# Optimization experiments

Measured on AMD Instinct MI355X. Metric: run time of the kernel, lower is better.

The kernel has to match this reference:

```python
import jax, jax.numpy as jnp
import numpy as np

H = 64; H2 = 32; B = 256; NPART = 64
NP = B * NPART          # 16384 part nodes
PER_TF = 512            # torque/force nodes per graph
NT = B * PER_TF; NF = NT
E = 262144              # edges per edge type
L = 5; T = 4            # 4 main hetero layers + 1 actor layer; 4 edge types
NEG = 0.2; EPS = 1e-5


def _seg_softmax(e, seg, n):
    # softmax over entries sharing the same segment id (along axis 0)
    m = jax.lax.stop_gradient(jax.ops.segment_max(e, seg, num_segments=n))
    ex = jnp.exp(e - m[seg])
    s = jax.ops.segment_sum(ex, seg, num_segments=n)
    return ex / s[seg]


def _gat(x_s, x_d, es, ed, Ws, Wd, a_s, a_d, b, n_dst):
    # PyG GATConv, heads=1, add_self_loops=False, bipartite (x_src, x_dst)
    hs = x_s @ Ws                      # [Ns,H]
    hd = x_d @ Wd                      # [Nd,H]
    e = jax.nn.leaky_relu((hs @ a_s)[es] + (hd @ a_d)[ed], NEG)   # [E]
    al = _seg_softmax(e, ed, n_dst)                                # attn per dst neighborhood
    return jax.ops.segment_sum(al[:, None] * hs[es], ed, num_segments=n_dst) + b


def _hetero_layer(xp, xt, xf, edges, Ws, Wd, a_s, a_d, b):
    # to_hetero(aggr='sum'): one GATConv per edge type, sum into each dst type
    (pts, ptd), (tps, tpd), (pfs, pfd), (fps, fpd) = edges
    out_t = _gat(xp, xt, pts, ptd, Ws[0], Wd[0], a_s[0], a_d[0], b[0], xt.shape[0])
    out_p = (_gat(xt, xp, tps, tpd, Ws[1], Wd[1], a_s[1], a_d[1], b[1], xp.shape[0])
             + _gat(xf, xp, fps, fpd, Ws[3], Wd[3], a_s[3], a_d[3], b[3], xp.shape[0]))
    out_f = _gat(xp, xf, pfs, pfd, Ws[2], Wd[2], a_s[2], a_d[2], b[2], xf.shape[0])
    return out_p, out_t, out_f


def _pool(x):
    # MultiAggregation([max, min, mean]); segments are uniform -> reshape
    xr = x.reshape(B, -1, x.shape[-1])
    return jnp.concatenate([xr.max(1), xr.min(1), xr.mean(1)], axis=-1)


def reference(mass, part_state, torque_x, force_x,
              e_pt_src, e_pt_dst, e_tp_src, e_tp_dst,
              e_pf_src, e_pf_dst, e_fp_src, e_fp_dst,
              batch, part_id,
              emb_parts_W, emb_state, W_src, W_dst, a_src, a_dst, b_conv,
              ln_gamma, ln_beta, out_a_W, out_a_b,
              innet_W, innet_b, full_W, full_b, outnet_W, outnet_b):
    edges = ((e_pt_src, e_pt_dst), (e_tp_src, e_tp_dst),
             (e_pf_src, e_pf_dst), (e_fp_src, e_fp_dst))
    idx = part_state[:, 0] + 2 * part_state[:, 1]
    xp = jnp.concatenate([mass @ emb_parts_W, emb_state[idx]], axis=-1)  # [NP,H]
    xt, xf = torque_x, force_x
    for l in range(4):  # main hetero GAT, ReLU between layers, none after last
        xp, xt, xf = _hetero_layer(xp, xt, xf, edges,
                                   W_src[l], W_dst[l], a_src[l], a_dst[l], b_conv[l])
        if l < 3:
            xp, xt, xf = jax.nn.relu(xp), jax.nn.relu(xt), jax.nn.relu(xf)
    # actor: 1-layer hetero GAT (no activation)
    ap, at, af = _hetero_layer(xp, xt, xf, edges,
                               W_src[4], W_dst[4], a_src[4], a_dst[4], b_conv[4])
    # node LayerNorm
    mu = ap.mean(-1, keepdims=True)
    var = ((ap - mu) ** 2).mean(-1, keepdims=True)
    ra = (ap - mu) / jnp.sqrt(var + EPS) * ln_gamma + ln_beta
    ra = ra @ out_a_W + out_a_b                         # [NP,2]
    soft = _seg_softmax(ra, batch, B)                   # softmax per graph, per channel
    actions = jnp.zeros((B, 2, NPART), dtype=ra.dtype).at[batch, :, part_id].set(soft)
    actions = actions.reshape(B, 2 * NPART)
    rep = jnp.concatenate([_pool(xp), _pool(xt), _pool(xf)], axis=1)   # [B, 9H]
    repV = jax.nn.gelu(rep @ innet_W + innet_b, approximate=False)
    repV = jax.nn.gelu(repV @ full_W + full_b, approximate=False)
    V = jnp.tanh(repV @ outnet_W + outnet_b)            # [B,1]
    return actions, V


def setup_inputs():
    key = jax.random.key(0)
    ks = iter(jax.random.split(key, 40))
    f32 = jnp.float32
    inp = {}
    inp['mass'] = jax.random.uniform(next(ks), (NP, 1), dtype=f32)
    inp['part_state'] = jax.random.randint(next(ks), (NP, 2), 0, 2, dtype=jnp.int32)
    inp['torque_x'] = jax.random.normal(next(ks), (NT, H), dtype=f32)
    inp['force_x'] = jax.random.normal(next(ks), (NF, H), dtype=f32)
    for name, n in [('e_pt_src', NP), ('e_pt_dst', NT), ('e_tp_src', NT), ('e_tp_dst', NP),
                    ('e_pf_src', NP), ('e_pf_dst', NF), ('e_fp_src', NF), ('e_fp_dst', NP)]:
        inp[name] = jax.random.randint(next(ks), (E,), 0, n, dtype=jnp.int32)
    inp['batch'] = (jnp.arange(NP) // NPART).astype(jnp.int32)
    inp['part_id'] = (jnp.arange(NP) % NPART).astype(jnp.int32)
    s = 1.0 / np.sqrt(H)
    inp['emb_parts_W'] = jax.random.normal(next(ks), (1, H2), dtype=f32)
    inp['emb_state'] = jax.random.normal(next(ks), (4, H2), dtype=f32)
    inp['W_src'] = jax.random.normal(next(ks), (L, T, H, H), dtype=f32) * s
    inp['W_dst'] = jax.random.normal(next(ks), (L, T, H, H), dtype=f32) * s
    inp['a_src'] = jax.random.normal(next(ks), (L, T, H), dtype=f32) * s
    inp['a_dst'] = jax.random.normal(next(ks), (L, T, H), dtype=f32) * s
    inp['b_conv'] = jax.random.normal(next(ks), (L, T, H), dtype=f32) * 0.01
    inp['ln_gamma'] = jnp.ones((H,), dtype=f32)
    inp['ln_beta'] = jnp.zeros((H,), dtype=f32)
    inp['out_a_W'] = jax.random.normal(next(ks), (H, 2), dtype=f32) * s
    inp['out_a_b'] = jnp.zeros((2,), dtype=f32)
    inp['innet_W'] = jax.random.normal(next(ks), (9 * H, H), dtype=f32) / np.sqrt(9.0 * H)
    inp['innet_b'] = jnp.zeros((H,), dtype=f32)
    inp['full_W'] = jax.random.normal(next(ks), (H, H), dtype=f32) * s
    inp['full_b'] = jnp.zeros((H,), dtype=f32)
    inp['outnet_W'] = jax.random.normal(next(ks), (H, 1), dtype=f32) * s
    inp['outnet_b'] = jnp.zeros((1,), dtype=f32)
    return inp
```

## Files before the change

kernel.cpp:

```cpp
#include <hip/hip_runtime.h>
#include <math.h>

#define NP_ 16384
#define NT_ 131072
#define NF_ 131072
#define E_  262144
#define B_  256
#define NDTOT 294912
#define E4_  1048576

#define D0 0
#define D1 131072
#define D2 147456
#define D3 278528
#define S0 0
#define S1 16384
#define S2 147456
#define S3 163840

typedef float v4f __attribute__((ext_vector_type(4)));

__device__ __forceinline__ float dot4(float4 a, float4 b) {
  return a.x * b.x + a.y * b.y + a.z * b.z + a.w * b.w;
}

__device__ __forceinline__ void nt_store4(float* p, float4 o) {
  v4f v = { o.x, o.y, o.z, o.w };
  __builtin_nontemporal_store(v, (v4f*)p);
}

__device__ __forceinline__ float4 gather_row(int kb, int ke, float ad,
    const int* __restrict__ sortsrc, const float* __restrict__ aS_seg,
    const float* __restrict__ xsrc, int q, int lanebase, float* si_out) {
  float4 acc = make_float4(0.f, 0.f, 0.f, 0.f);
  float m = -3e38f, ssum = 0.f;
  for (int base = kb; base < ke; base += 16) {
    int k = base + q;
    int valid = (k < ke);
    int sidx = valid ? sortsrc[k] : 0;
    float e = -3e38f;
    if (valid) {
      e = aS_seg[sidx] + ad;
      e = e > 0.f ? e : 0.2f * e;
    }
    float cm = e;
#pragma unroll
    for (int off = 1; off < 16; off <<= 1) cm = fmaxf(cm, __shfl_xor(cm, off));
    float mn = fmaxf(m, cm);
    float w = valid ? __expf(e - mn) : 0.f;
    float ws = w;
#pragma unroll
    for (int off = 1; off < 16; off <<= 1) ws += __shfl_xor(ws, off);
    float r = __expf(m - mn);
    ssum = ssum * r + ws;
    acc.x *= r; acc.y *= r; acc.z *= r; acc.w *= r;
    int cnt = min(16, ke - base);
    int i = 0;
    for (; i + 4 <= cnt; i += 4) {
      float w0 = __shfl(w, lanebase + i, 64);
      float w1 = __shfl(w, lanebase + i + 1, 64);
      float w2 = __shfl(w, lanebase + i + 2, 64);
      float w3 = __shfl(w, lanebase + i + 3, 64);
      int s0 = __shfl(sidx, lanebase + i, 64);
      int s1 = __shfl(sidx, lanebase + i + 1, 64);
      int s2 = __shfl(sidx, lanebase + i + 2, 64);
      int s3 = __shfl(sidx, lanebase + i + 3, 64);
      float4 x0 = *(const float4*)(xsrc + (size_t)s0 * 64 + q * 4);
      float4 x1 = *(const float4*)(xsrc + (size_t)s1 * 64 + q * 4);
      float4 x2 = *(const float4*)(xsrc + (size_t)s2 * 64 + q * 4);
      float4 x3 = *(const float4*)(xsrc + (size_t)s3 * 64 + q * 4);
      acc.x += w0 * x0.x + w1 * x1.x + w2 * x2.x + w3 * x3.x;
      acc.y += w0 * x0.y + w1 * x1.y + w2 * x2.y + w3 * x3.y;
      acc.z += w0 * x0.z + w1 * x1.z + w2 * x2.z + w3 * x3.z;
      acc.w += w0 * x0.w + w1 * x1.w + w2 * x2.w + w3 * x3.w;
    }
    for (; i < cnt; i++) {
      float wi = __shfl(w, lanebase + i, 64);
      int si = __shfl(sidx, lanebase + i, 64);
      float4 xv = *(const float4*)(xsrc + (size_t)si * 64 + q * 4);
      acc.x += wi * xv.x; acc.y += wi * xv.y; acc.z += wi * xv.z; acc.w += wi * xv.w;
    }
    m = mn;
  }
  *si_out = (ssum > 0.f) ? 1.f / ssum : 0.f;
  return acc;
}

__global__ void k_wa(const float* __restrict__ Wsrc, const float* __restrict__ Wdst,
                     const float* __restrict__ asrc, const float* __restrict__ adst,
                     float* __restrict__ wsas, float* __restrict__ wdad) {
  int b = blockIdx.x;
  int lt = b >> 1;
  int role = b & 1;
  int k = threadIdx.x;
  const float* W = (role == 0 ? Wsrc : Wdst) + ((size_t)(lt * 64 + k)) * 64;
  const float* a = (role == 0 ? asrc : adst) + lt * 64;
  float s = 0.f;
  for (int i = 0; i < 64; i++) s += W[i] * a[i];
  (role == 0 ? wsas : wdad)[lt * 64 + k] = s;
}

__global__ __launch_bounds__(256) void k_build_xp(const float* __restrict__ mass,
    const int* __restrict__ ps, const float* __restrict__ embW,
    const float* __restrict__ embS, const float* __restrict__ wsas,
    const float* __restrict__ wdad, float* __restrict__ xp,
    float* __restrict__ aS, float* __restrict__ aD) {
  int tid = threadIdx.x;
  int n = blockIdx.x * 16 + (tid >> 4);
  int q = tid & 15;
  float4 v;
  if (q < 8) {
    float mv = mass[n];
    const float* e = embW + q * 4;
    v.x = mv * e[0]; v.y = mv * e[1]; v.z = mv * e[2]; v.w = mv * e[3];
  } else {
    int idx = ps[n * 2] + 2 * ps[n * 2 + 1];
    const float4* e = (const float4*)(embS + idx * 32 + (q - 8) * 4);
    v = *e;
  }
  *(float4*)(xp + (size_t)n * 64 + q * 4) = v;
  float4 w0 = *(const float4*)(wsas + 0 * 64 + q * 4);
  float4 w2 = *(const float4*)(wsas + 2 * 64 + q * 4);
  float4 d1 = *(const float4*)(wdad + 1 * 64 + q * 4);
  float4 d3 = *(const float4*)(wdad + 3 * 64 + q * 4);
  float p0 = dot4(v, w0), p2 = dot4(v, w2), p1 = dot4(v, d1), p3 = dot4(v, d3);
#pragma unroll
  for (int off = 1; off < 16; off <<= 1) {
    p0 += __shfl_xor(p0, off); p2 += __shfl_xor(p2, off);
    p1 += __shfl_xor(p1, off); p3 += __shfl_xor(p3, off);
  }
  if (q == 0) { aS[S0 + n] = p0; aS[S2 + n] = p2; aD[D1 + n] = p1; aD[D3 + n] = p3; }
}

__global__ __launch_bounds__(256) void k_init_dots(const float* __restrict__ tx,
    const float* __restrict__ fx, const float* __restrict__ wsas,
    const float* __restrict__ wdad, float* __restrict__ aS, float* __restrict__ aD) {
  int tid = threadIdx.x;
  int q = tid & 15, slot = tid >> 4;
  int b = blockIdx.x;
  int isF = (b >= 8192);
  int n = (isF ? b - 8192 : b) * 16 + slot;
  const float* src = (isF ? fx : tx) + (size_t)n * 64 + q * 4;
  float4 v = *(const float4*)src;
  int tsrc = isF ? 3 : 1, tdst = isF ? 2 : 0;
  float4 ws = *(const float4*)(wsas + tsrc * 64 + q * 4);
  float4 wd = *(const float4*)(wdad + tdst * 64 + q * 4);
  float pS = dot4(v, ws), pD = dot4(v, wd);
#pragma unroll
  for (int off = 1; off < 16; off <<= 1) {
    pS += __shfl_xor(pS, off); pD += __shfl_xor(pD, off);
  }
  if (q == 0) {
    if (!isF) { aS[S1 + n] = pS; aD[D0 + n] = pD; }
    else      { aS[S3 + n] = pS; aD[D2 + n] = pD; }
  }
}

__global__ __launch_bounds__(256) void k_count(
    const int* __restrict__ d0, const int* __restrict__ d1,
    const int* __restrict__ d2, const int* __restrict__ d3,
    int* __restrict__ counts) {
  __shared__ int cnt[64];
  int b = blockIdx.x;
  int t = b >> 6, c = b & 63;
  const int* dp = (t == 0) ? d0 : (t == 1) ? d1 : (t == 2) ? d2 : d3;
  int sh = (t & 1) ? 8 : 11;
  int tid = threadIdx.x;
  if (tid < 64) cnt[tid] = 0;
  __syncthreads();
  const int4* dp4 = (const int4*)dp + (size_t)c * 1024;
  for (int i = tid; i < 1024; i += 256) {
    int4 v = dp4[i];
    atomicAdd(&cnt[v.x >> sh], 1);
    atomicAdd(&cnt[v.y >> sh], 1);
    atomicAdd(&cnt[v.z >> sh], 1);
    atomicAdd(&cnt[v.w >> sh], 1);
  }
  __syncthreads();
  if (tid < 64) counts[(b << 6) + tid] = cnt[tid];
}

__global__ __launch_bounds__(256) void k_bases(const int* __restrict__ counts,
    int* __restrict__ cbase, int* __restrict__ granBase, int* __restrict__ rowptr) {
  __shared__ int tot[256];
  int tid = threadIdx.x;
  int t = tid >> 6, g = tid & 63;
  int s = 0;
  for (int c = 0; c < 64; c++) s += counts[(((t << 6) | c) << 6) + g];
  tot[tid] = s;
  __syncthreads();
  for (int off = 1; off < 256; off <<= 1) {
    int x = 0; if (tid >= off) x = tot[tid - off];
    __syncthreads(); tot[tid] += x; __syncthreads();
  }
  int gb = tot[tid] - s;
  granBase[tid] = gb;
  if (tid == 255) granBase[256] = E4_;
  if (tid == 0) rowptr[NDTOT] = E4_;
  int run = gb;
  for (int c = 0; c < 64; c++) {
    int idx = (((t << 6) | c) << 6) + g;
    int v = counts[idx];
    cbase[idx] = run;
    run += v;
  }
}

__global__ __launch_bounds__(256) void k_place(
    const int* __restrict__ d0, const int* __restrict__ s0,
    const int* __restrict__ d1, const int* __restrict__ s1,
    const int* __restrict__ d2, const int* __restrict__ s2,
    const int* __restrict__ d3, const int* __restrict__ s3,
    const int* __restrict__ cbase, int2* __restrict__ pairs) {
  __shared__ int cur[64];
  int b = blockIdx.x;
  int t = b >> 6, c = b & 63;
  const int* dp; const int* sp;
  if (t == 0) { dp = d0; sp = s0; }
  else if (t == 1) { dp = d1; sp = s1; }
  else if (t == 2) { dp = d2; sp = s2; }
  else { dp = d3; sp = s3; }
  int sh = (t & 1) ? 8 : 11;
  int tid = threadIdx.x;
  if (tid < 64) cur[tid] = cbase[(b << 6) + tid];
  __syncthreads();
  const int4* dp4 = (const int4*)dp + (size_t)c * 1024;
  const int4* sp4 = (const int4*)sp + (size_t)c * 1024;
  for (int i = tid; i < 1024; i += 256) {
    int4 d = dp4[i];
    int4 s = sp4[i];
    int pos;
    pos = atomicAdd(&cur[d.x >> sh], 1); pairs[pos] = make_int2(d.x, s.x);
    pos = atomicAdd(&cur[d.y >> sh], 1); pairs[pos] = make_int2(d.y, s.y);
    pos = atomicAdd(&cur[d.z >> sh], 1); pairs[pos] = make_int2(d.z, s.z);
    pos = atomicAdd(&cur[d.w >> sh], 1); pairs[pos] = make_int2(d.w, s.w);
  }
}

__global__ __launch_bounds__(256) void k_build(const int2* __restrict__ pairs,
    const int* __restrict__ granBase, int* __restrict__ rowptr,
    int* __restrict__ sortsrc) {
  __shared__ int cnt[2048];
  __shared__ int psum[256];
  int g = blockIdx.x;
  int t = g >> 6, gg = g & 63;
  int rows = (t & 1) ? 256 : 2048;
  int rowLo = gg * rows;
  int csr0;
  if (t == 0) csr0 = D0 + rowLo;
  else if (t == 1) csr0 = D1 + rowLo;
  else if (t == 2) csr0 = D2 + rowLo;
  else csr0 = D3 + rowLo;
  int eb = granBase[g], ee = granBase[g + 1];
  int tid = threadIdx.x;
  for (int i = tid; i < rows; i += 256) cnt[i] = 0;
  __syncthreads();
  for (int i = eb + tid; i < ee; i += 256) {
    int2 p = pairs[i];
    atomicAdd(&cnt[p.x - rowLo], 1);
  }
  __syncthreads();
  int per = rows >> 8;
  int b0 = tid * per;
  int s = 0;
  for (int j = 0; j < per; j++) s += cnt[b0 + j];
  psum[tid] = s;
  __syncthreads();
  for (int off = 1; off < 256; off <<= 1) {
    int x = 0; if (tid >= off) x = psum[tid - off];
    __syncthreads(); psum[tid] += x; __syncthreads();
  }
  int run = psum[tid] - s;
  for (int j = 0; j < per; j++) {
    int v = cnt[b0 + j];
    cnt[b0 + j] = run;
    rowptr[csr0 + b0 + j] = eb + run;
    run += v;
  }
  __syncthreads();
  for (int i = eb + tid; i < ee; i += 256) {
    int2 p = pairs[i];
    int pos = eb + atomicAdd(&cnt[p.x - rowLo], 1);
    sortsrc[pos] = p.y;
  }
}

__global__ __launch_bounds__(256) void k_part_hs(int l, const float* __restrict__ Wsrc,
    const float* __restrict__ bconv, const float* __restrict__ xt,
    const float* __restrict__ xf, const float* __restrict__ xp,
    const int* __restrict__ rowptr, const int* __restrict__ sortsrc,
    const float* __restrict__ aSrd, const float* __restrict__ aDrd,
    float* __restrict__ aSwr, float* __restrict__ aDwr,
    const float* __restrict__ wsas, const float* __restrict__ wdad,
    float* __restrict__ xpo, float* __restrict__ hs0, float* __restrict__ hs2,
    int relu, int writeDots) {
  __shared__ float Wl[4096];
  __shared__ float shC[2176];
  int tid = threadIdx.x;

  if (blockIdx.x >= NP_ / 16) {
    int b = blockIdx.x - NP_ / 16;
    const float4* W0g = (const float4*)(Wsrc + (size_t)(l * 4 + 0) * 4096);
    const float4* W2g = (const float4*)(Wsrc + (size_t)(l * 4 + 2) * 4096);
#pragma unroll
    for (int i = 0; i < 4; i++) ((float4*)Wl)[i * 256 + tid] = W0g[i * 256 + tid];
    int rlocal = tid >> 4, q = tid & 15;
    int n = b * 16 + rlocal;
    float4 xv = *(const float4*)(xp + (size_t)n * 64 + q * 4);
    *(float4*)(shC + rlocal * 68 + q * 4) = xv;
    __syncthreads();
    const float* xr = shC + rlocal * 68;
    const float4* Wc = (const float4*)Wl;
    float4 o0 = make_float4(0.f, 0.f, 0.f, 0.f);
#pragma unroll 4
    for (int k4 = 0; k4 < 16; k4++) {
      float4 a4 = *(const float4*)(xr + k4 * 4);
#pragma unroll
      for (int kk = 0; kk < 4; kk++) {
        float av = kk == 0 ? a4.x : kk == 1 ? a4.y : kk == 2 ? a4.z : a4.w;
        float4 w0 = Wc[(k4 * 4 + kk) * 16 + q];
        o0.x += av * w0.x; o0.y += av * w0.y; o0.z += av * w0.z; o0.w += av * w0.w;
      }
    }
    *(float4*)(hs0 + (size_t)n * 64 + q * 4) = o0;
    __syncthreads();
#pragma unroll
    for (int i = 0; i < 4; i++) ((float4*)Wl)[i * 256 + tid] = W2g[i * 256 + tid];
    __syncthreads();
    float4 o2 = make_float4(0.f, 0.f, 0.f, 0.f);
#pragma unroll 4
    for (int k4 = 0; k4 < 16; k4++) {
      float4 a4 = *(const float4*)(xr + k4 * 4);
#pragma unroll
      for (int kk = 0; kk < 4; kk++) {
        float av = kk == 0 ? a4.x : kk == 1 ? a4.y : kk == 2 ? a4.z : a4.w;
        float4 w2 = Wc[(k4 * 4 + kk) * 16 + q];
        o2.x += av * w2.x; o2.y += av * w2.y; o2.z += av * w2.z; o2.w += av * w2.w;
      }
    }
    *(float4*)(hs2 + (size_t)n * 64 + q * 4) = o2;
    return;
  }

  float* rowA = shC; float* rowB = shC + 1088;
  const float4* W1g = (const float4*)(Wsrc + (size_t)(l * 4 + 1) * 4096);
  const float4* W3g = (const float4*)(Wsrc + (size_t)(l * 4 + 3) * 4096);
#pragma unroll
  for (int i = 0; i < 4; i++) ((float4*)Wl)[i * 256 + tid] = W1g[i * 256 + tid];

  int rlocal = tid >> 4;
  int q = tid & 15;
  int lanebase = (tid & 63) & 48;
  int n = blockIdx.x * 16 + rlocal;
  int row1 = D1 + n;
  int row3 = D3 + n;

  {
    int kb = rowptr[row1], ke = rowptr[row1 + 1];
    float si;
    float4 acc = gather_row(kb, ke, aDrd[row1], sortsrc, aSrd + S1, xt, q, lanebase, &si);
    acc.x *= si; acc.y *= si; acc.z *= si; acc.w *= si;
    *(float4*)(rowA + rlocal * 68 + q * 4) = acc;
  }
  {
    int kb = rowptr[row3], ke = rowptr[row3 + 1];
    float si;
    float4 acc = gather_row(kb, ke, aDrd[row3], sortsrc, aSrd + S3, xf, q, lanebase, &si);
    acc.x *= si; acc.y *= si; acc.z *= si; acc.w *= si;
    *(float4*)(rowB + rlocal * 68 + q * 4) = acc;
  }
  __syncthreads();

  const float* b1 = bconv + (l * 4 + 1) * 64;
  const float* b3 = bconv + (l * 4 + 3) * 64;
  float4 o = *(const float4*)(b1 + q * 4);
  float4 o3b = *(const float4*)(b3 + q * 4);
  o.x += o3b.x; o.y += o3b.y; o.z += o3b.z; o.w += o3b.w;
  const float4* Wc = (const float4*)Wl;
#pragma unroll 4
  for (int k4 = 0; k4 < 16; k4++) {
    float4 a4 = *(const float4*)(rowA + rlocal * 68 + k4 * 4);
#pragma unroll
    for (int kk = 0; kk < 4; kk++) {
      float av = kk == 0 ? a4.x : kk == 1 ? a4.y : kk == 2 ? a4.z : a4.w;
      float4 w1 = Wc[(k4 * 4 + kk) * 16 + q];
      o.x += av * w1.x; o.y += av * w1.y; o.z += av * w1.z; o.w += av * w1.w;
    }
  }
  __syncthreads();
#pragma unroll
  for (int i = 0; i < 4; i++) ((float4*)Wl)[i * 256 + tid] = W3g[i * 256 + tid];
  __syncthreads();
#pragma unroll 4
  for (int k4 = 0; k4 < 16; k4++) {
    float4 b4 = *(const float4*)(rowB + rlocal * 68 + k4 * 4);
#pragma unroll
    for (int kk = 0; kk < 4; kk++) {
      float bv = kk == 0 ? b4.x : kk == 1 ? b4.y : kk == 2 ? b4.z : b4.w;
      float4 w3 = Wc[(k4 * 4 + kk) * 16 + q];
      o.x += bv * w3.x; o.y += bv * w3.y; o.z += bv * w3.z; o.w += bv * w3.w;
    }
  }
  if (relu) { o.x = fmaxf(o.x, 0.f); o.y = fmaxf(o.y, 0.f); o.z = fmaxf(o.z, 0.f); o.w = fmaxf(o.w, 0.f); }
  nt_store4(xpo + (size_t)n * 64 + q * 4, o);

  if (writeDots) {
    float4 w0 = *(const float4*)(wsas + (size_t)((l + 1) * 4 + 0) * 64 + q * 4);
    float4 w2 = *(const float4*)(wsas + (size_t)((l + 1) * 4 + 2) * 64 + q * 4);
    float4 d1 = *(const float4*)(wdad + (size_t)((l + 1) * 4 + 1) * 64 + q * 4);
    float4 d3 = *(const float4*)(wdad + (size_t)((l + 1) * 4 + 3) * 64 + q * 4);
    float p0 = dot4(o, w0), p2 = dot4(o, w2), p1 = dot4(o, d1), p3 = dot4(o, d3);
#pragma unroll
    for (int off = 1; off < 16; off <<= 1) {
      p0 += __shfl_xor(p0, off); p2 += __shfl_xor(p2, off);
      p1 += __shfl_xor(p1, off); p3 += __shfl_xor(p3, off);
    }
    if (q == 0) { aSwr[S0 + n] = p0; aSwr[S2 + n] = p2; aDwr[D1 + n] = p1; aDwr[D3 + n] = p3; }
  }
}

__global__ __launch_bounds__(256) void k_tf(int l, const float* __restrict__ hs0,
    const float* __restrict__ hs2, const float* __restrict__ bconv,
    const int* __restrict__ rowptr, const int* __restrict__ sortsrc,
    const float* __restrict__ aSrd, const float* __restrict__ aDrd,
    float* __restrict__ aSwr, float* __restrict__ aDwr,
    const float* __restrict__ wsas, const float* __restrict__ wdad,
    float* __restrict__ xt, float* __restrict__ xf, int relu) {
  int tid = threadIdx.x;
  int q = tid & 15, slot = tid >> 4;
  int b = blockIdx.x;
  int isF = (b >= 8192);
  int rg = ((isF ? b - 8192 : b) * 16 + slot);
  int csr = (isF ? D2 : D0) + rg;
  const float* hs = isF ? hs2 : hs0;
  const float* aSseg = aSrd + (isF ? S2 : S0);
  int t = isF ? 2 : 0;

  int kb = rowptr[csr], ke = rowptr[csr + 1];
  float ad = aDrd[csr];
  float m = -3e38f, ssum = 0.f;
  float4 acc = make_float4(0.f, 0.f, 0.f, 0.f);
  for (int k = kb; k < ke; k++) {
    int sidx = sortsrc[k];
    const float4* xv4 = (const float4*)(hs + (size_t)sidx * 64 + q * 4);
    float e = aSseg[sidx] + ad;
    e = e > 0.f ? e : 0.2f * e;
    float mn = fmaxf(m, e);
    float r = __expf(m - mn);
    float w = __expf(e - mn);
    float4 xv = *xv4;
    ssum = ssum * r + w;
    acc.x = acc.x * r + w * xv.x;
    acc.y = acc.y * r + w * xv.y;
    acc.z = acc.z * r + w * xv.z;
    acc.w = acc.w * r + w * xv.w;
    m = mn;
  }
  float si = (ssum > 0.f) ? 1.f / ssum : 0.f;

  float4 bias = *(const float4*)(bconv + (size_t)(l * 4 + t) * 64 + q * 4);
  float4 o;
  o.x = acc.x * si + bias.x; o.y = acc.y * si + bias.y;
  o.z = acc.z * si + bias.z; o.w = acc.w * si + bias.w;
  if (relu) {
    o.x = fmaxf(o.x, 0.f); o.y = fmaxf(o.y, 0.f);
    o.z = fmaxf(o.z, 0.f); o.w = fmaxf(o.w, 0.f);
  }
  nt_store4((isF ? xf : xt) + (size_t)rg * 64 + q * 4, o);

  int tsrc = isF ? 3 : 1, tdst = isF ? 2 : 0;
  float4 wsv = *(const float4*)(wsas + (size_t)((l + 1) * 4 + tsrc) * 64 + q * 4);
  float4 wdv = *(const float4*)(wdad + (size_t)((l + 1) * 4 + tdst) * 64 + q * 4);
  float pS = dot4(o, wsv);
  float pD = dot4(o, wdv);
#pragma unroll
  for (int off = 1; off < 16; off <<= 1) {
    pS += __shfl_xor(pS, off); pD += __shfl_xor(pD, off);
  }
  if (q == 0) {
    if (!isF) { aSwr[S1 + rg] = pS; aDwr[D0 + rg] = pD; }
    else      { aSwr[S3 + rg] = pS; aDwr[D2 + rg] = pD; }
  }
}

__global__ __launch_bounds__(256) void k_actor(const float* __restrict__ ap,
    const float* __restrict__ gamma, const float* __restrict__ beta,
    const float* __restrict__ oaW, const float* __restrict__ oab,
    float* __restrict__ outp) {
  __shared__ float r0s[64], r1s[64];
  int g = blockIdx.x;
  int wave = threadIdx.x >> 6, lane = threadIdx.x & 63;
  float gl = gamma[lane], bl = beta[lane];
  float w0 = oaW[lane * 2], w1 = oaW[lane * 2 + 1];
  float ob0 = oab[0], ob1 = oab[1];
  for (int i = 0; i < 16; i++) {
    int n = g * 64 + wave * 16 + i;
    float v = ap[(size_t)n * 64 + lane];
    float s = v;
    for (int off = 32; off > 0; off >>= 1) s += __shfl_xor(s, off);
    float mean = s * (1.f / 64.f);
    float d = v - mean;
    float s2 = d * d;
    for (int off = 32; off > 0; off >>= 1) s2 += __shfl_xor(s2, off);
    float var = s2 * (1.f / 64.f);
    float y = d / sqrtf(var + 1e-5f) * gl + bl;
    float p0 = y * w0, p1 = y * w1;
    for (int off = 32; off > 0; off >>= 1) { p0 += __shfl_xor(p0, off); p1 += __shfl_xor(p1, off); }
    if (lane == 0) { r0s[wave * 16 + i] = p0 + ob0; r1s[wave * 16 + i] = p1 + ob1; }
  }
  __syncthreads();
  if (threadIdx.x < 64) {
    int p = threadIdx.x;
    float r0 = r0s[p], r1 = r1s[p];
    float m0 = r0, m1 = r1;
    for (int off = 32; off > 0; off >>= 1) {
      m0 = fmaxf(m0, __shfl_xor(m0, off));
      m1 = fmaxf(m1, __shfl_xor(m1, off));
    }
    float e0 = __expf(r0 - m0), e1 = __expf(r1 - m1);
    float s0 = e0, s1 = e1;
    for (int off = 32; off > 0; off >>= 1) { s0 += __shfl_xor(s0, off); s1 += __shfl_xor(s1, off); }
    outp[g * 128 + p] = e0 / s0;
    outp[g * 128 + 64 + p] = e1 / s1;
  }
}

__global__ __launch_bounds__(256) void k_pool(const float* __restrict__ xp,
    const float* __restrict__ xt, const float* __restrict__ xf,
    float* __restrict__ pool) {
  __shared__ float pmax[4][64], pmin[4][64], psum[4][64];
  int b = blockIdx.x;
  int g = b / 9, c = b % 9;
  int tid = threadIdx.x;
  int grp = tid >> 6, col = tid & 63;
  const float* src; int R;
  if (c == 0)      { src = xp + (size_t)g * 64 * 64; R = 64; }
  else if (c <= 4) { src = xt + ((size_t)g * 512 + (size_t)(c - 1) * 128) * 64; R = 128; }
  else             { src = xf + ((size_t)g * 512 + (size_t)(c - 5) * 128) * 64; R = 128; }
  float mx = -3e38f, mn = 3e38f, sm = 0.f;
  for (int r = grp; r < R; r += 4) {
    float v = src[(size_t)r * 64 + col];
    mx = fmaxf(mx, v); mn = fminf(mn, v); sm += v;
  }
  pmax[grp][col] = mx; pmin[grp][col] = mn; psum[grp][col] = sm;
  __syncthreads();
  if (grp == 0) {
    float M = fmaxf(fmaxf(pmax[0][col], pmax[1][col]), fmaxf(pmax[2][col], pmax[3][col]));
    float m = fminf(fminf(pmin[0][col], pmin[1][col]), fminf(pmin[2][col], pmin[3][col]));
    float S = psum[0][col] + psum[1][col] + psum[2][col] + psum[3][col];
    float* o = pool + ((size_t)(g * 9 + c) * 3) * 64;
    o[col] = M; o[64 + col] = m; o[128 + col] = S;
  }
}

__global__ __launch_bounds__(256) void k_vhead(const float* __restrict__ pool,
    const float* __restrict__ inW, const float* __restrict__ inb,
    const float* __restrict__ fW, const float* __restrict__ fb,
    const float* __restrict__ oW, const float* __restrict__ ob,
    float* __restrict__ outV) {
  __shared__ float rep[576];
  __shared__ float red[256];
  __shared__ float h1[64];
  int g = blockIdx.x, tid = threadIdx.x;
  if (tid < 64) {
    int col = tid;
    const float* pg = pool + (size_t)g * 9 * 3 * 64;
    rep[col] = pg[col];
    rep[64 + col] = pg[64 + col];
    rep[128 + col] = pg[128 + col] * (1.f / 64.f);
    float M = -3e38f, m = 3e38f, S = 0.f;
    for (int c = 1; c <= 4; c++) {
      const float* p = pg + (size_t)c * 192;
      M = fmaxf(M, p[col]); m = fminf(m, p[64 + col]); S += p[128 + col];
    }
    rep[192 + col] = M; rep[256 + col] = m; rep[320 + col] = S * (1.f / 512.f);
    M = -3e38f; m = 3e38f; S = 0.f;
    for (int c = 5; c <= 8; c++) {
      const float* p = pg + (size_t)c * 192;
      M = fmaxf(M, p[col]); m = fminf(m, p[64 + col]); S += p[128 + col];
    }
    rep[384 + col] = M; rep[448 + col] = m; rep[512 + col] = S * (1.f / 512.f);
  }
  __syncthreads();
  const float ISQ2 = 0.70710678118654752f;
  {
    int j = tid & 63, p = tid >> 6;
    float s = 0.f;
    for (int k = p * 144; k < (p + 1) * 144; k++) s += rep[k] * inW[k * 64 + j];
    red[tid] = s;
  }
  __syncthreads();
  if (tid < 64) {
    float s = red[tid] + red[64 + tid] + red[128 + tid] + red[192 + tid] + inb[tid];
    h1[tid] = 0.5f * s * (1.f + erff(s * ISQ2));
  }
  __syncthreads();
  if (tid < 64) {
    float s = fb[tid];
    for (int k = 0; k < 64; k++) s += h1[k] * fW[k * 64 + tid];
    float h2 = 0.5f * s * (1.f + erff(s * ISQ2));
    float p = h2 * oW[tid];
    for (int off = 32; off > 0; off >>= 1) p += __shfl_xor(p, off);
    if (tid == 0) outV[g] = tanhf(p + ob[0]);
  }
}

extern "C" void kernel_launch(void* const* d_in, const int* in_sizes, int n_in,
                              void* d_out, int out_size, void* d_ws, size_t ws_size,
                              hipStream_t stream) {
  (void)in_sizes; (void)n_in; (void)out_size; (void)ws_size;
  const float* mass = (const float*)d_in[0];
  const int*   ps   = (const int*)d_in[1];
  const float* torque_x = (const float*)d_in[2];
  const float* force_x  = (const float*)d_in[3];
  const int* ept_s = (const int*)d_in[4];  const int* ept_d = (const int*)d_in[5];
  const int* etp_s = (const int*)d_in[6];  const int* etp_d = (const int*)d_in[7];
  const int* epf_s = (const int*)d_in[8];  const int* epf_d = (const int*)d_in[9];
  const int* efp_s = (const int*)d_in[10]; const int* efp_d = (const int*)d_in[11];
  const float* embW  = (const float*)d_in[14];
  const float* embS  = (const float*)d_in[15];
  const float* Wsrc  = (const float*)d_in[16];
  const float* Wdst  = (const float*)d_in[17];
  const float* asrc  = (const float*)d_in[18];
  const float* adst  = (const float*)d_in[19];
  const float* bconv = (const float*)d_in[20];
  const float* gamma = (const float*)d_in[21];
  const float* beta  = (const float*)d_in[22];
  const float* oaW   = (const float*)d_in[23];
  const float* oab   = (const float*)d_in[24];
  const float* inW   = (const float*)d_in[25];
  const float* inb   = (const float*)d_in[26];
  const float* fW    = (const float*)d_in[27];
  const float* fb    = (const float*)d_in[28];
  const float* oW    = (const float*)d_in[29];
  const float* ob    = (const float*)d_in[30];

  char* base = (char*)d_ws;
  size_t off = 0;
  auto alloc = [&](size_t bytes) -> void* {
    void* r = base + off;
    off = (off + bytes + 255) & ~(size_t)255;
    return r;
  };
  float* xp0 = (float*)alloc((size_t)NP_ * 64 * 4);
  float* xp1 = (float*)alloc((size_t)NP_ * 64 * 4);
  float* xt  = (float*)alloc((size_t)NT_ * 64 * 4);
  float* xf  = (float*)alloc((size_t)NF_ * 64 * 4);
  float* hs0 = (float*)alloc((size_t)NP_ * 64 * 4);
  float* hs2 = (float*)alloc((size_t)NP_ * 64 * 4);
  float* aSb[2], *aDb[2];
  aSb[0] = (float*)alloc((size_t)NDTOT * 4);
  aSb[1] = (float*)alloc((size_t)NDTOT * 4);
  aDb[0] = (float*)alloc((size_t)NDTOT * 4);
  aDb[1] = (float*)alloc((size_t)NDTOT * 4);
  float* wsas = (float*)alloc(1280 * 4);
  float* wdad = (float*)alloc(1280 * 4);
  float* pool = (float*)alloc((size_t)B_ * 9 * 3 * 64 * 4);
  int* rowptr = (int*)alloc((size_t)(NDTOT + 1) * 4);
  int* sortsrc = (int*)alloc((size_t)E4_ * 4);
  int2* pairs  = (int2*)alloc((size_t)E4_ * 8);
  int* counts  = (int*)alloc(16384 * 4);
  int* cbase   = (int*)alloc(16384 * 4);
  int* granBase = (int*)alloc(257 * 4);

  k_wa<<<40, 64, 0, stream>>>(Wsrc, Wdst, asrc, adst, wsas, wdad);
  k_build_xp<<<NP_ / 16, 256, 0, stream>>>(mass, ps, embW, embS, wsas, wdad,
                                           xp0, aSb[0], aDb[0]);
  k_init_dots<<<(NT_ + NF_) / 16, 256, 0, stream>>>(torque_x, force_x,
                                                    wsas, wdad, aSb[0], aDb[0]);
  k_count<<<256, 256, 0, stream>>>(ept_d, etp_d, epf_d, efp_d, counts);
  k_bases<<<1, 256, 0, stream>>>(counts, cbase, granBase, rowptr);
  k_place<<<256, 256, 0, stream>>>(ept_d, ept_s, etp_d, etp_s, epf_d, epf_s,
                                   efp_d, efp_s, cbase, pairs);
  k_build<<<256, 256, 0, stream>>>(pairs, granBase, rowptr, sortsrc);

  float* xpbuf[2] = { xp0, xp1 };
  int cur = 0;
  for (int l = 0; l < 5; l++) {
    int ri = l & 1, wi = (l + 1) & 1;
    int relu = (l < 3) ? 1 : 0;
    const float* xtr = (l == 0) ? torque_x : xt;
    const float* xfr = (l == 0) ? force_x : xf;
    int grid = (l < 4) ? (2 * NP_ / 16) : (NP_ / 16);
    k_part_hs<<<grid, 256, 0, stream>>>(l, Wsrc, bconv, xtr, xfr, xpbuf[cur],
                                        rowptr, sortsrc,
                                        aSb[ri], aDb[ri], aSb[wi], aDb[wi],
                                        wsas, wdad, xpbuf[1 - cur], hs0, hs2,
                                        relu, (l < 4) ? 1 : 0);
    if (l < 4)
      k_tf<<<(NT_ + NF_) / 16, 256, 0, stream>>>(l, hs0, hs2, bconv, rowptr, sortsrc,
                                                 aSb[ri], aDb[ri], aSb[wi], aDb[wi],
                                                 wsas, wdad, xt, xf, relu);
    cur = 1 - cur;
  }

  float* outp = (float*)d_out;
  k_actor<<<B_, 256, 0, stream>>>(xp1, gamma, beta, oaW, oab, outp);
  k_pool<<<B_ * 9, 256, 0, stream>>>(xp0, xt, xf, pool);
  k_vhead<<<B_, 256, 0, stream>>>(pool, inW, inb, fW, fb, oW, ob, outp + B_ * 128);
}
```

Before: 593.6 us.

## Fuse part and torque/force GAT passes into one kernel per layer

The separate part-update and torque/force-update kernels are merged into a single k_layer launch per layer. Part blocks compute the next layer's hs0/hs2 projections in their epilogue, and the tf blocks read the previous layer's hs buffers. This lets both node groups run concurrently in one grid, removing one launch and the serialisation between them per layer, and drops the xp round trip for early layers. It costs double-buffered xt/xf/hs storage (the CSR build scratch is aliased into the spare buffers) and an extra two __syncthreads-bound matmuls in the part blocks.

```diff
diff --git a/kernel.cpp b/kernel.cpp
--- a/kernel.cpp
+++ b/kernel.cpp
@@ -100,14 +100,17 @@
   (role == 0 ? wsas : wdad)[lt * 64 + k] = s;
 }
 
-__global__ __launch_bounds__(256) void k_build_xp(const float* __restrict__ mass,
+__global__ __launch_bounds__(256) void k_build_xp_hs(const float* __restrict__ mass,
     const int* __restrict__ ps, const float* __restrict__ embW,
-    const float* __restrict__ embS, const float* __restrict__ wsas,
-    const float* __restrict__ wdad, float* __restrict__ xp,
+    const float* __restrict__ embS, const float* __restrict__ Wsrc,
+    const float* __restrict__ wsas, const float* __restrict__ wdad,
+    float* __restrict__ hs0, float* __restrict__ hs2,
     float* __restrict__ aS, float* __restrict__ aD) {
+  __shared__ float Wl[4096];
+  __shared__ float xl[16 * 68];
   int tid = threadIdx.x;
-  int n = blockIdx.x * 16 + (tid >> 4);
-  int q = tid & 15;
+  int rlocal = tid >> 4, q = tid & 15;
+  int n = blockIdx.x * 16 + rlocal;
   float4 v;
   if (q < 8) {
     float mv = mass[n];
@@ -115,10 +118,9 @@
     v.x = mv * e[0]; v.y = mv * e[1]; v.z = mv * e[2]; v.w = mv * e[3];
   } else {
     int idx = ps[n * 2] + 2 * ps[n * 2 + 1];
-    const float4* e = (const float4*)(embS + idx * 32 + (q - 8) * 4);
-    v = *e;
-  }
-  *(float4*)(xp + (size_t)n * 64 + q * 4) = v;
+    v = *(const float4*)(embS + idx * 32 + (q - 8) * 4);
+  }
+  *(float4*)(xl + rlocal * 68 + q * 4) = v;
   float4 w0 = *(const float4*)(wsas + 0 * 64 + q * 4);
   float4 w2 = *(const float4*)(wsas + 2 * 64 + q * 4);
   float4 d1 = *(const float4*)(wdad + 1 * 64 + q * 4);
@@ -130,6 +132,41 @@
     p1 += __shfl_xor(p1, off); p3 += __shfl_xor(p3, off);
   }
   if (q == 0) { aS[S0 + n] = p0; aS[S2 + n] = p2; aD[D1 + n] = p1; aD[D3 + n] = p3; }
+  const float4* W0g = (const float4*)(Wsrc + (size_t)0 * 4096);
+  const float4* W2g = (const float4*)(Wsrc + (size_t)2 * 4096);
+#pragma unroll
+  for (int i = 0; i < 4; i++) ((float4*)Wl)[i * 256 + tid] = W0g[i * 256 + tid];
+  __syncthreads();
+  const float* xr = xl + rlocal * 68;
+  const float4* Wc = (const float4*)Wl;
+  float4 o0 = make_float4(0.f, 0.f, 0.f, 0.f);
+#pragma unroll 4
+  for (int k4 = 0; k4 < 16; k4++) {
+    float4 a4 = *(const float4*)(xr + k4 * 4);
+#pragma unroll
+    for (int kk = 0; kk < 4; kk++) {
+      float av = kk == 0 ? a4.x : kk == 1 ? a4.y : kk == 2 ? a4.z : a4.w;
+      float4 w = Wc[(k4 * 4 + kk) * 16 + q];
+      o0.x += av * w.x; o0.y += av * w.y; o0.z += av * w.z; o0.w += av * w.w;
+    }
+  }
+  *(float4*)(hs0 + (size_t)n * 64 + q * 4) = o0;
+  __syncthreads();
+#pragma unroll
+  for (int i = 0; i < 4; i++) ((float4*)Wl)[i * 256 + tid] = W2g[i * 256 + tid];
+  __syncthreads();
+  float4 o2 = make_float4(0.f, 0.f, 0.f, 0.f);
+#pragma unroll 4
+  for (int k4 = 0; k4 < 16; k4++) {
+    float4 a4 = *(const float4*)(xr + k4 * 4);
+#pragma unroll
+    for (int kk = 0; kk < 4; kk++) {
+      float av = kk == 0 ? a4.x : kk == 1 ? a4.y : kk == 2 ? a4.z : a4.w;
+      float4 w = Wc[(k4 * 4 + kk) * 16 + q];
+      o2.x += av * w.x; o2.y += av * w.y; o2.z += av * w.z; o2.w += av * w.w;
+    }
+  }
+  *(float4*)(hs2 + (size_t)n * 64 + q * 4) = o2;
 }
 
 __global__ __launch_bounds__(256) void k_init_dots(const float* __restrict__ tx,
@@ -140,8 +177,7 @@
   int b = blockIdx.x;
   int isF = (b >= 8192);
   int n = (isF ? b - 8192 : b) * 16 + slot;
-  const float* src = (isF ? fx : tx) + (size_t)n * 64 + q * 4;
-  float4 v = *(const float4*)src;
+  float4 v = *(const float4*)((isF ? fx : tx) + (size_t)n * 64 + q * 4);
   int tsrc = isF ? 3 : 1, tdst = isF ? 2 : 0;
   float4 ws = *(const float4*)(wsas + tsrc * 64 + q * 4);
   float4 wd = *(const float4*)(wdad + tdst * 64 + q * 4);
@@ -285,60 +321,75 @@
   }
 }
 
-__global__ __launch_bounds__(256) void k_part_hs(int l, const float* __restrict__ Wsrc,
-    const float* __restrict__ bconv, const float* __restrict__ xt,
-    const float* __restrict__ xf, const float* __restrict__ xp,
+__global__ __launch_bounds__(256) void k_layer(int l, const float* __restrict__ Wsrc,
+    const float* __restrict__ bconv, const float* __restrict__ xtR,
+    const float* __restrict__ xfR,
     const int* __restrict__ rowptr, const int* __restrict__ sortsrc,
     const float* __restrict__ aSrd, const float* __restrict__ aDrd,
     float* __restrict__ aSwr, float* __restrict__ aDwr,
     const float* __restrict__ wsas, const float* __restrict__ wdad,
-    float* __restrict__ xpo, float* __restrict__ hs0, float* __restrict__ hs2,
-    int relu, int writeDots) {
+    const float* __restrict__ hs0R, const float* __restrict__ hs2R,
+    float* __restrict__ hs0W, float* __restrict__ hs2W,
+    float* __restrict__ xtW, float* __restrict__ xfW,
+    float* __restrict__ xpo, int relu, int doHsNext, int writeXp, int writeDots) {
   __shared__ float Wl[4096];
   __shared__ float shC[2176];
   int tid = threadIdx.x;
 
   if (blockIdx.x >= NP_ / 16) {
     int b = blockIdx.x - NP_ / 16;
-    const float4* W0g = (const float4*)(Wsrc + (size_t)(l * 4 + 0) * 4096);
-    const float4* W2g = (const float4*)(Wsrc + (size_t)(l * 4 + 2) * 4096);
-#pragma unroll
-    for (int i = 0; i < 4; i++) ((float4*)Wl)[i * 256 + tid] = W0g[i * 256 + tid];
-    int rlocal = tid >> 4, q = tid & 15;
-    int n = b * 16 + rlocal;
-    float4 xv = *(const float4*)(xp + (size_t)n * 64 + q * 4);
-    *(float4*)(shC + rlocal * 68 + q * 4) = xv;
-    __syncthreads();
-    const float* xr = shC + rlocal * 68;
-    const float4* Wc = (const float4*)Wl;
-    float4 o0 = make_float4(0.f, 0.f, 0.f, 0.f);
-#pragma unroll 4
-    for (int k4 = 0; k4 < 16; k4++) {
-      float4 a4 = *(const float4*)(xr + k4 * 4);
-#pragma unroll
-      for (int kk = 0; kk < 4; kk++) {
-        float av = kk == 0 ? a4.x : kk == 1 ? a4.y : kk == 2 ? a4.z : a4.w;
-        float4 w0 = Wc[(k4 * 4 + kk) * 16 + q];
-        o0.x += av * w0.x; o0.y += av * w0.y; o0.z += av * w0.z; o0.w += av * w0.w;
-      }
-    }
-    *(float4*)(hs0 + (size_t)n * 64 + q * 4) = o0;
-    __syncthreads();
-#pragma unroll
-    for (int i = 0; i < 4; i++) ((float4*)Wl)[i * 256 + tid] = W2g[i * 256 + tid];
-    __syncthreads();
-    float4 o2 = make_float4(0.f, 0.f, 0.f, 0.f);
-#pragma unroll 4
-    for (int k4 = 0; k4 < 16; k4++) {
-      float4 a4 = *(const float4*)(xr + k4 * 4);
-#pragma unroll
-      for (int kk = 0; kk < 4; kk++) {
-        float av = kk == 0 ? a4.x : kk == 1 ? a4.y : kk == 2 ? a4.z : a4.w;
-        float4 w2 = Wc[(k4 * 4 + kk) * 16 + q];
-        o2.x += av * w2.x; o2.y += av * w2.y; o2.z += av * w2.z; o2.w += av * w2.w;
-      }
-    }
-    *(float4*)(hs2 + (size_t)n * 64 + q * 4) = o2;
+    int q = tid & 15, slot = tid >> 4;
+    int isF = (b >= 8192);
+    int rg = ((isF ? b - 8192 : b) * 16 + slot);
+    int csr = (isF ? D2 : D0) + rg;
+    const float* hs = isF ? hs2R : hs0R;
+    const float* aSseg = aSrd + (isF ? S2 : S0);
+    int t = isF ? 2 : 0;
+
+    int kb = rowptr[csr], ke = rowptr[csr + 1];
+    float ad = aDrd[csr];
+    float m = -3e38f, ssum = 0.f;
+    float4 acc = make_float4(0.f, 0.f, 0.f, 0.f);
+    for (int k = kb; k < ke; k++) {
+      int sidx = sortsrc[k];
+      const float4* xv4 = (const float4*)(hs + (size_t)sidx * 64 + q * 4);
+      float e = aSseg[sidx] + ad;
+      e = e > 0.f ? e : 0.2f * e;
+      float mn = fmaxf(m, e);
+      float r = __expf(m - mn);
+      float w = __expf(e - mn);
+      float4 xv = *xv4;
+      ssum = ssum * r + w;
+      acc.x = acc.x * r + w * xv.x;
+      acc.y = acc.y * r + w * xv.y;
+      acc.z = acc.z * r + w * xv.z;
+      acc.w = acc.w * r + w * xv.w;
+      m = mn;
+    }
+    float si = (ssum > 0.f) ? 1.f / ssum : 0.f;
+    float4 bias = *(const float4*)(bconv + (size_t)(l * 4 + t) * 64 + q * 4);
+    float4 o;
+    o.x = acc.x * si + bias.x; o.y = acc.y * si + bias.y;
+    o.z = acc.z * si + bias.z; o.w = acc.w * si + bias.w;
+    if (relu) {
+      o.x = fmaxf(o.x, 0.f); o.y = fmaxf(o.y, 0.f);
+      o.z = fmaxf(o.z, 0.f); o.w = fmaxf(o.w, 0.f);
+    }
+    nt_store4((isF ? xfW : xtW) + (size_t)rg * 64 + q * 4, o);
+
+    int tsrc = isF ? 3 : 1, tdst = isF ? 2 : 0;
+    float4 wsv = *(const float4*)(wsas + (size_t)((l + 1) * 4 + tsrc) * 64 + q * 4);
+    float4 wdv = *(const float4*)(wdad + (size_t)((l + 1) * 4 + tdst) * 64 + q * 4);
+    float pS = dot4(o, wsv);
+    float pD = dot4(o, wdv);
+#pragma unroll
+    for (int off = 1; off < 16; off <<= 1) {
+      pS += __shfl_xor(pS, off); pD += __shfl_xor(pD, off);
+    }
+    if (q == 0) {
+      if (!isF) { aSwr[S1 + rg] = pS; aDwr[D0 + rg] = pD; }
+      else      { aSwr[S3 + rg] = pS; aDwr[D2 + rg] = pD; }
+    }
     return;
   }
 
@@ -358,14 +409,14 @@
   {
     int kb = rowptr[row1], ke = rowptr[row1 + 1];
     float si;
-    float4 acc = gather_row(kb, ke, aDrd[row1], sortsrc, aSrd + S1, xt, q, lanebase, &si);
+    float4 acc = gather_row(kb, ke, aDrd[row1], sortsrc, aSrd + S1, xtR, q, lanebase, &si);
     acc.x *= si; acc.y *= si; acc.z *= si; acc.w *= si;
     *(float4*)(rowA + rlocal * 68 + q * 4) = acc;
   }
   {
     int kb = rowptr[row3], ke = rowptr[row3 + 1];
     float si;
-    float4 acc = gather_row(kb, ke, aDrd[row3], sortsrc, aSrd + S3, xf, q, lanebase, &si);
+    float4 acc = gather_row(kb, ke, aDrd[row3], sortsrc, aSrd + S3, xfR, q, lanebase, &si);
     acc.x *= si; acc.y *= si; acc.z *= si; acc.w *= si;
     *(float4*)(rowB + rlocal * 68 + q * 4) = acc;
   }
@@ -402,7 +453,7 @@
     }
   }
   if (relu) { o.x = fmaxf(o.x, 0.f); o.y = fmaxf(o.y, 0.f); o.z = fmaxf(o.z, 0.f); o.w = fmaxf(o.w, 0.f); }
-  nt_store4(xpo + (size_t)n * 64 + q * 4, o);
+  if (writeXp) nt_store4(xpo + (size_t)n * 64 + q * 4, o);
 
   if (writeDots) {
     float4 w0 = *(const float4*)(wsas + (size_t)((l + 1) * 4 + 0) * 64 + q * 4);
@@ -417,69 +468,43 @@
     }
     if (q == 0) { aSwr[S0 + n] = p0; aSwr[S2 + n] = p2; aDwr[D1 + n] = p1; aDwr[D3 + n] = p3; }
   }
-}
-
-__global__ __launch_bounds__(256) void k_tf(int l, const float* __restrict__ hs0,
-    const float* __restrict__ hs2, const float* __restrict__ bconv,
-    const int* __restrict__ rowptr, const int* __restrict__ sortsrc,
-    const float* __restrict__ aSrd, const float* __restrict__ aDrd,
-    float* __restrict__ aSwr, float* __restrict__ aDwr,
-    const float* __restrict__ wsas, const float* __restrict__ wdad,
-    float* __restrict__ xt, float* __restrict__ xf, int relu) {
-  int tid = threadIdx.x;
-  int q = tid & 15, slot = tid >> 4;
-  int b = blockIdx.x;
-  int isF = (b >= 8192);
-  int rg = ((isF ? b - 8192 : b) * 16 + slot);
-  int csr = (isF ? D2 : D0) + rg;
-  const float* hs = isF ? hs2 : hs0;
-  const float* aSseg = aSrd + (isF ? S2 : S0);
-  int t = isF ? 2 : 0;
-
-  int kb = rowptr[csr], ke = rowptr[csr + 1];
-  float ad = aDrd[csr];
-  float m = -3e38f, ssum = 0.f;
-  float4 acc = make_float4(0.f, 0.f, 0.f, 0.f);
-  for (int k = kb; k < ke; k++) {
-    int sidx = sortsrc[k];
-    const float4* xv4 = (const float4*)(hs + (size_t)sidx * 64 + q * 4);
-    float e = aSseg[sidx] + ad;
-    e = e > 0.f ? e : 0.2f * e;
-    float mn = fmaxf(m, e);
-    float r = __expf(m - mn);
-    float w = __expf(e - mn);
-    float4 xv = *xv4;
-    ssum = ssum * r + w;
-    acc.x = acc.x * r + w * xv.x;
-    acc.y = acc.y * r + w * xv.y;
-    acc.z = acc.z * r + w * xv.z;
-    acc.w = acc.w * r + w * xv.w;
-    m = mn;
-  }
-  float si = (ssum > 0.f) ? 1.f / ssum : 0.f;
-
-  float4 bias = *(const float4*)(bconv + (size_t)(l * 4 + t) * 64 + q * 4);
-  float4 o;
-  o.x = acc.x * si + bias.x; o.y = acc.y * si + bias.y;
-  o.z = acc.z * si + bias.z; o.w = acc.w * si + bias.w;
-  if (relu) {
-    o.x = fmaxf(o.x, 0.f); o.y = fmaxf(o.y, 0.f);
-    o.z = fmaxf(o.z, 0.f); o.w = fmaxf(o.w, 0.f);
-  }
-  nt_store4((isF ? xf : xt) + (size_t)rg * 64 + q * 4, o);
-
-  int tsrc = isF ? 3 : 1, tdst = isF ? 2 : 0;
-  float4 wsv = *(const float4*)(wsas + (size_t)((l + 1) * 4 + tsrc) * 64 + q * 4);
-  float4 wdv = *(const float4*)(wdad + (size_t)((l + 1) * 4 + tdst) * 64 + q * 4);
-  float pS = dot4(o, wsv);
-  float pD = dot4(o, wdv);
-#pragma unroll
-  for (int off = 1; off < 16; off <<= 1) {
-    pS += __shfl_xor(pS, off); pD += __shfl_xor(pD, off);
-  }
-  if (q == 0) {
-    if (!isF) { aSwr[S1 + rg] = pS; aDwr[D0 + rg] = pD; }
-    else      { aSwr[S3 + rg] = pS; aDwr[D2 + rg] = pD; }
+
+  if (doHsNext) {
+    const float4* W0n = (const float4*)(Wsrc + (size_t)((l + 1) * 4 + 0) * 4096);
+    const float4* W2n = (const float4*)(Wsrc + (size_t)((l + 1) * 4 + 2) * 4096);
+    *(float4*)(rowA + rlocal * 68 + q * 4) = o;
+    __syncthreads();
+#pragma unroll
+    for (int i = 0; i < 4; i++) ((float4*)Wl)[i * 256 + tid] = W0n[i * 256 + tid];
+    __syncthreads();
+    float4 h0 = make_float4(0.f, 0.f, 0.f, 0.f);
+#pragma unroll 4
+    for (int k4 = 0; k4 < 16; k4++) {
+      float4 a4 = *(const float4*)(rowA + rlocal * 68 + k4 * 4);
+#pragma unroll
+      for (int kk = 0; kk < 4; kk++) {
+        float av = kk == 0 ? a4.x : kk == 1 ? a4.y : kk == 2 ? a4.z : a4.w;
+        float4 w = Wc[(k4 * 4 + kk) * 16 + q];
+        h0.x += av * w.x; h0.y += av * w.y; h0.z += av * w.z; h0.w += av * w.w;
+      }
+    }
+    *(float4*)(hs0W + (size_t)n * 64 + q * 4) = h0;
+    __syncthreads();
+#pragma unroll
+    for (int i = 0; i < 4; i++) ((float4*)Wl)[i * 256 + tid] = W2n[i * 256 + tid];
+    __syncthreads();
+    float4 h2 = make_float4(0.f, 0.f, 0.f, 0.f);
+#pragma unroll 4
+    for (int k4 = 0; k4 < 16; k4++) {
+      float4 a4 = *(const float4*)(rowA + rlocal * 68 + k4 * 4);
+#pragma unroll
+      for (int kk = 0; kk < 4; kk++) {
+        float av = kk == 0 ? a4.x : kk == 1 ? a4.y : kk == 2 ? a4.z : a4.w;
+        float4 w = Wc[(k4 * 4 + kk) * 16 + q];
+        h2.x += av * w.x; h2.y += av * w.y; h2.z += av * w.z; h2.w += av * w.w;
+      }
+    }
+    *(float4*)(hs2W + (size_t)n * 64 + q * 4) = h2;
   }
 }
 
@@ -642,12 +667,18 @@
     off = (off + bytes + 255) & ~(size_t)255;
     return r;
   };
-  float* xp0 = (float*)alloc((size_t)NP_ * 64 * 4);
-  float* xp1 = (float*)alloc((size_t)NP_ * 64 * 4);
-  float* xt  = (float*)alloc((size_t)NT_ * 64 * 4);
-  float* xf  = (float*)alloc((size_t)NF_ * 64 * 4);
-  float* hs0 = (float*)alloc((size_t)NP_ * 64 * 4);
-  float* hs2 = (float*)alloc((size_t)NP_ * 64 * 4);
+  float* xp4 = (float*)alloc((size_t)NP_ * 64 * 4);
+  float* xp5 = (float*)alloc((size_t)NP_ * 64 * 4);
+  float* xtb[2]; float* xfb[2];
+  xtb[0] = (float*)alloc((size_t)NT_ * 64 * 4);
+  xfb[0] = (float*)alloc((size_t)NF_ * 64 * 4);
+  xtb[1] = (float*)alloc((size_t)NT_ * 64 * 4);
+  xfb[1] = (float*)alloc((size_t)NF_ * 64 * 4);
+  float* hs0b[2]; float* hs2b[2];
+  hs0b[0] = (float*)alloc((size_t)NP_ * 64 * 4);
+  hs0b[1] = (float*)alloc((size_t)NP_ * 64 * 4);
+  hs2b[0] = (float*)alloc((size_t)NP_ * 64 * 4);
+  hs2b[1] = (float*)alloc((size_t)NP_ * 64 * 4);
   float* aSb[2], *aDb[2];
   aSb[0] = (float*)alloc((size_t)NDTOT * 4);
   aSb[1] = (float*)alloc((size_t)NDTOT * 4);
@@ -658,14 +689,15 @@
   float* pool = (float*)alloc((size_t)B_ * 9 * 3 * 64 * 4);
   int* rowptr = (int*)alloc((size_t)(NDTOT + 1) * 4);
   int* sortsrc = (int*)alloc((size_t)E4_ * 4);
-  int2* pairs  = (int2*)alloc((size_t)E4_ * 8);
-  int* counts  = (int*)alloc(16384 * 4);
-  int* cbase   = (int*)alloc(16384 * 4);
-  int* granBase = (int*)alloc(257 * 4);
+  int2* pairs  = (int2*)xtb[1];
+  int* counts  = (int*)xfb[1];
+  int* cbase   = counts + 16384;
+  int* granBase = cbase + 16384;
 
   k_wa<<<40, 64, 0, stream>>>(Wsrc, Wdst, asrc, adst, wsas, wdad);
-  k_build_xp<<<NP_ / 16, 256, 0, stream>>>(mass, ps, embW, embS, wsas, wdad,
-                                           xp0, aSb[0], aDb[0]);
+  k_build_xp_hs<<<NP_ / 16, 256, 0, stream>>>(mass, ps, embW, embS, Wsrc,
+                                              wsas, wdad, hs0b[0], hs2b[0],
+                                              aSb[0], aDb[0]);
   k_init_dots<<<(NT_ + NF_) / 16, 256, 0, stream>>>(torque_x, force_x,
                                                     wsas, wdad, aSb[0], aDb[0]);
   k_count<<<256, 256, 0, stream>>>(ept_d, etp_d, epf_d, efp_d, counts);
@@ -674,28 +706,29 @@
                                    efp_d, efp_s, cbase, pairs);
   k_build<<<256, 256, 0, stream>>>(pairs, granBase, rowptr, sortsrc);
 
-  float* xpbuf[2] = { xp0, xp1 };
-  int cur = 0;
   for (int l = 0; l < 5; l++) {
     int ri = l & 1, wi = (l + 1) & 1;
     int relu = (l < 3) ? 1 : 0;
-    const float* xtr = (l == 0) ? torque_x : xt;
-    const float* xfr = (l == 0) ? force_x : xf;
-    int grid = (l < 4) ? (2 * NP_ / 16) : (NP_ / 16);
-    k_part_hs<<<grid, 256, 0, stream>>>(l, Wsrc, bconv, xtr, xfr, xpbuf[cur],
-                                        rowptr, sortsrc,
-                                        aSb[ri], aDb[ri], aSb[wi], aDb[wi],
-                                        wsas, wdad, xpbuf[1 - cur], hs0, hs2,
-                                        relu, (l < 4) ? 1 : 0);
-    if (l < 4)
-      k_tf<<<(NT_ + NF_) / 16, 256, 0, stream>>>(l, hs0, hs2, bconv, rowptr, sortsrc,
-                                                 aSb[ri], aDb[ri], aSb[wi], aDb[wi],
-                                                 wsas, wdad, xt, xf, relu);
-    cur = 1 - cur;
+    const float* xtR = (l == 0) ? torque_x : xtb[(l - 1) & 1];
+    const float* xfR = (l == 0) ? force_x : xfb[(l - 1) & 1];
+    float* xtW = xtb[l & 1];
+    float* xfW = xfb[l & 1];
+    int doTf = (l < 4);
+    int doHsNext = (l < 3);
+    int writeXp = (l >= 3);
+    float* xpo = (l == 3) ? xp4 : ((l == 4) ? xp5 : (float*)0);
+    int grid = (NP_ / 16) + (doTf ? 16384 : 0);
+    k_layer<<<grid, 256, 0, stream>>>(l, Wsrc, bconv, xtR, xfR, rowptr, sortsrc,
+                                      aSb[ri], aDb[ri], aSb[wi], aDb[wi],
+                                      wsas, wdad,
+                                      hs0b[l & 1], hs2b[l & 1],
+                                      hs0b[(l + 1) & 1], hs2b[(l + 1) & 1],
+                                      xtW, xfW, xpo, relu, doHsNext, writeXp,
+                                      (l < 4) ? 1 : 0);
   }
 
   float* outp = (float*)d_out;
-  k_actor<<<B_, 256, 0, stream>>>(xp1, gamma, beta, oaW, oab, outp);
-  k_pool<<<B_ * 9, 256, 0, stream>>>(xp0, xt, xf, pool);
+  k_actor<<<B_, 256, 0, stream>>>(xp5, gamma, beta, oaW, oab, outp);
+  k_pool<<<B_ * 9, 256, 0, stream>>>(xp4, xtb[1], xfb[1], pool);
   k_vhead<<<B_, 256, 0, stream>>>(pool, inW, inb, fW, fb, oW, ob, outp + B_ * 128);
 }
```

After: 679.8 us. 14.5% more time.
